# Optimization experiments

Hardware: AMD Instinct MI355X
Metric: run time of the kernel (lower is better)

## Reference

```python
import jax, jax.numpy as jnp
import numpy as np

HEADS = 4
HEAD_DIM = 32
WS = (8, 8)  # window size (h, w)


def _rel_bias_indices():
    idx = np.array([[i, j] for i in range(WS[0]) for j in range(WS[1])])  # [64,2]
    rel = idx[None, :, :] - idx[:, None, :]                               # [64,64,2]
    rel[:, :, 0] += WS[0] - 1
    rel[:, :, 1] += WS[1] - 1
    return rel

_REL = _rel_bias_indices()


def setup_inputs() -> dict:
    key = jax.random.key(0)
    ks = jax.random.split(key, 7)
    dim = 128
    inner = HEADS * HEAD_DIM
    return {
        "x": jax.random.normal(ks[0], (16, 128, 128, dim), dtype=jnp.float32),
        "w_qkv": jax.random.normal(ks[1], (dim, 3 * inner), dtype=jnp.float32) * 0.02,
        "w_out": jax.random.normal(ks[2], (inner, dim), dtype=jnp.float32) * 0.02,
        "b_out": jnp.zeros((dim,), dtype=jnp.float32),
        "pos_embedding": jax.random.normal(ks[3], (2 * WS[0] - 1, 2 * WS[1] - 1), dtype=jnp.float32) * 0.02,
        "ul_mask": jax.random.normal(ks[4], (WS[0] * WS[1], WS[0] * WS[1]), dtype=jnp.float32) * 0.02,
        "lr_mask": jax.random.normal(ks[5], (WS[0] * WS[1], WS[0] * WS[1]), dtype=jnp.float32) * 0.02,
    }


def _window_split(t, b, nw_h, nw_w):
    # (b, n_h, n_w, h*d) -> (b, h, nw, ws^2, d)
    t = t.reshape(b, nw_h, WS[0], nw_w, WS[1], HEADS, HEAD_DIM)
    t = t.transpose(0, 5, 1, 3, 2, 4, 6)
    return t.reshape(b, HEADS, nw_h * nw_w, WS[0] * WS[1], HEAD_DIM)


def reference(x, w_qkv, w_out, b_out, pos_embedding, ul_mask, lr_mask):
    b, n_h, n_w, _ = x.shape
    nw_h, nw_w = n_h // WS[0], n_w // WS[1]
    scale = HEAD_DIM ** -0.5
    disp = (WS[0] // 2, WS[1] // 2)

    # cyclic shift (torch.roll with shifts -ws//2)
    xs = jnp.roll(x, (-disp[0], -disp[1]), axis=(1, 2))

    qkv = xs @ w_qkv  # (b, n_h, n_w, 3*inner)
    q, k, v = jnp.split(qkv, 3, axis=-1)
    q = _window_split(q, b, nw_h, nw_w)
    k = _window_split(k, b, nw_h, nw_w)
    v = _window_split(v, b, nw_h, nw_w)

    dots = jnp.einsum('bhwid,bhwjd->bhwij', q, k) * scale
    bias = pos_embedding[_REL[:, :, 0], _REL[:, :, 1]]  # [64,64]
    dots = dots + bias
    # shift masks: bottom row of windows and last column of windows
    dots = dots.at[:, :, -nw_w:].add(ul_mask)
    dots = dots.at[:, :, nw_w - 1::nw_w].add(lr_mask)

    attn = jax.nn.softmax(dots, axis=-1)
    out = jnp.einsum('bhwij,bhwjd->bhwid', attn, v)

    # (b, h, nw, ws^2, d) -> (b, n_h, n_w, h*d)
    out = out.reshape(b, HEADS, nw_h, nw_w, WS[0], WS[1], HEAD_DIM)
    out = out.transpose(0, 2, 4, 3, 5, 1, 6).reshape(b, n_h, n_w, HEADS * HEAD_DIM)

    out = out @ w_out + b_out
    out = jnp.roll(out, (disp[0], disp[1]), axis=(1, 2))  # cyclic back shift
    return out
```

## Files before the change

kernel.cpp:

```cpp
#include <hip/hip_runtime.h>


typedef __bf16 bf16x8 __attribute__((ext_vector_type(8)));
typedef short  s16x8  __attribute__((ext_vector_type(8)));
typedef float  f32x4  __attribute__((ext_vector_type(4)));

static __device__ __forceinline__ float bf2f(unsigned short u) {
  unsigned x = ((unsigned)u) << 16;
  return __builtin_bit_cast(float, x);
}
static __device__ __forceinline__ unsigned short f2bf(float f) {
  unsigned x = __builtin_bit_cast(unsigned, f);
  x += 0x7FFFu + ((x >> 16) & 1u);
  return (unsigned short)(x >> 16);
}
static __device__ __forceinline__ f32x4 mfma16(s16x8 a, s16x8 b, f32x4 c) {
  return __builtin_amdgcn_mfma_f32_16x16x32_bf16(
      __builtin_bit_cast(bf16x8, a), __builtin_bit_cast(bf16x8, b), c, 0, 0, 0);
}
static __device__ __forceinline__ void bar_lds() {
  __builtin_amdgcn_sched_barrier(0);
  asm volatile("s_waitcnt lgkmcnt(0)" ::: "memory");
  __builtin_amdgcn_s_barrier();
  __builtin_amdgcn_sched_barrier(0);
}

__global__ void prep_weights(const float* __restrict__ wqkv,
                             const float* __restrict__ wout,
                             unsigned short* __restrict__ wqkvT,
                             unsigned short* __restrict__ woutT) {
  int idx = blockIdx.x * blockDim.x + threadIdx.x;
  const int total1 = 384 * 128;
  if (idx < total1) {
    int n = idx >> 7, k = idx & 127;
    wqkvT[idx] = f2bf(wqkv[k * 384 + n]);
  } else {
    int i2 = idx - total1;
    int n = i2 >> 7, k = i2 & 127;
    woutT[i2] = f2bf(wout[k * 128 + n]);
  }
}

#define OFF_XS  0
#define OFF_Q   17408
#define OFF_K   34816
#define OFF_V   52224
#define OFF_S   70656
#define OFF_OA  107520
#define OFF_BI  124928
#define SMEM_SZ 141568

#define BATCH_STRIDE (128 * 128 * 128)

__global__ __launch_bounds__(1024, 4)
void swin_fused(const float* __restrict__ x,
                const unsigned short* __restrict__ wqkvT,
                const unsigned short* __restrict__ woutT,
                const float* __restrict__ b_out,
                const float* __restrict__ pe,
                const float* __restrict__ ulm,
                const float* __restrict__ lrm,
                float* __restrict__ out) {
  __shared__ __align__(16) unsigned char smem[SMEM_SZ];
  unsigned short* xs_s   = (unsigned short*)(smem + OFF_XS);
  unsigned short* q_s    = (unsigned short*)(smem + OFF_Q);
  unsigned short* k_s    = (unsigned short*)(smem + OFF_K);
  unsigned short* v_s    = (unsigned short*)(smem + OFF_V);
  unsigned short* S_s    = (unsigned short*)(smem + OFF_S);
  float*          osr_s  = (float*)(smem + OFF_S);
  unsigned short* oa_s   = (unsigned short*)(smem + OFF_OA);
  float*          bias_s = (float*)(smem + OFF_BI);

  const int tid  = threadIdx.x;
  const int lane = tid & 63;
  const int wave = tid >> 6;
  const int ln15 = lane & 15;
  const int quad = lane >> 4;
  const int m_sub = quad << 2;

  const int wh = blockIdx.x >> 4, ww = blockIdx.x & 15;

  const int tokA = tid >> 5, c4 = tid & 31;
  const int tokB = tokA + 32;
  const int giA = ((wh << 3) + (tokA >> 3) + 4) & 127;
  const int gjA = ((ww << 3) + (tokA & 7) + 4) & 127;
  const int giB = ((wh << 3) + (tokB >> 3) + 4) & 127;
  const int gjB = ((ww << 3) + (tokB & 7) + 4) & 127;
  const long offA = (long)(giA * 128 + gjA) * 128 + c4 * 4;
  const long offB = (long)(giB * 128 + gjB) * 128 + c4 * 4;
  const float* xA = x + offA;
  const float* xB = x + offB;

  {
    float4 a0 = *(const float4*)xA;
    float4 b0 = *(const float4*)xB;
    ushort4 pk;
    pk.x = f2bf(a0.x); pk.y = f2bf(a0.y); pk.z = f2bf(a0.z); pk.w = f2bf(a0.w);
    *(ushort4*)(xs_s + tokA * 136 + c4 * 4) = pk;
    pk.x = f2bf(b0.x); pk.y = f2bf(b0.y); pk.z = f2bf(b0.z); pk.w = f2bf(b0.w);
    *(ushort4*)(xs_s + tokB * 136 + c4 * 4) = pk;

    const bool has_ul = (wh == 15), has_lr = (ww == 15);
#pragma unroll
    for (int it = 0; it < 4; ++it) {
      int t = tid + it * 1024;
      int i = t >> 6, j = t & 63;
      int r0 = (j >> 3) - (i >> 3) + 7;
      int r1 = (j & 7) - (i & 7) + 7;
      float bsum = pe[r0 * 15 + r1];
      if (has_ul) bsum += ulm[t];
      if (has_lr) bsum += lrm[t];
      bias_s[i * 65 + j] = bsum;
    }
  }
  __syncthreads();

  for (int b = 0; b < 16; ++b) {
    float4 pfA, pfB;
    const bool pf = (b < 15);
    if (pf) {
      pfA = *(const float4*)(xA + (b + 1) * BATCH_STRIDE);
      pfB = *(const float4*)(xB + (b + 1) * BATCH_STRIDE);
    }
#pragma unroll
    for (int it = 0; it < 3; ++it) {
      int t  = wave + (it << 4);
      int nt = t >> 1, mh = t & 1;
      int n0 = nt << 4;
      int n  = n0 + ln15;
      const unsigned short* wp = wqkvT + n * 128 + quad * 8;
      s16x8 bfr[4];
#pragma unroll
      for (int ks = 0; ks < 4; ++ks) bfr[ks] = *(const s16x8*)(wp + ks * 32);
#pragma unroll
      for (int mi = 0; mi < 2; ++mi) {
        int mt = mh * 2 + mi;
        f32x4 acc = {0.f, 0.f, 0.f, 0.f};
#pragma unroll
        for (int ks = 0; ks < 4; ++ks) {
          s16x8 a = *(const s16x8*)(xs_s + (mt * 16 + ln15) * 136 + ks * 32 + quad * 8);
          acc = mfma16(a, bfr[ks], acc);
        }
        int tok0 = mt * 16 + m_sub;
        if (n0 < 128) {
#pragma unroll
          for (int r = 0; r < 4; ++r) q_s[(tok0 + r) * 136 + n] = f2bf(acc[r]);
        } else if (n0 < 256) {
          int nn = n - 128;
#pragma unroll
          for (int r = 0; r < 4; ++r) k_s[(tok0 + r) * 136 + nn] = f2bf(acc[r]);
        } else {
          int nn = n - 256;
          ushort4 pk;
          pk.x = f2bf(acc[0]); pk.y = f2bf(acc[1]);
          pk.z = f2bf(acc[2]); pk.w = f2bf(acc[3]);
          *(ushort4*)(v_s + nn * 72 + tok0) = pk;
        }
      }
    }
    bar_lds();

    {
      const int h  = wave >> 2;
      const int mt = wave & 3;
      unsigned short* Sh = S_s + h * 64 * 72;
      const int tok0 = mt * 16 + m_sub;
      s16x8 qf = *(const s16x8*)(q_s + (mt * 16 + ln15) * 136 + h * 32 + quad * 8);
      const float scale = 0.17677669529663687f;
      f32x4 sv[4];
#pragma unroll
      for (int nt = 0; nt < 4; ++nt) {
        s16x8 kf = *(const s16x8*)(k_s + (nt * 16 + ln15) * 136 + h * 32 + quad * 8);
        f32x4 acc = {0.f, 0.f, 0.f, 0.f};
        acc = mfma16(qf, kf, acc);
        int nn = nt * 16 + ln15;
#pragma unroll
        for (int r = 0; r < 4; ++r)
          sv[nt][r] = acc[r] * scale + bias_s[(tok0 + r) * 65 + nn];
      }

      if (pf) {
        ushort4 pk;
        pk.x = f2bf(pfA.x); pk.y = f2bf(pfA.y); pk.z = f2bf(pfA.z); pk.w = f2bf(pfA.w);
        *(ushort4*)(xs_s + tokA * 136 + c4 * 4) = pk;
        pk.x = f2bf(pfB.x); pk.y = f2bf(pfB.y); pk.z = f2bf(pfB.z); pk.w = f2bf(pfB.w);
        *(ushort4*)(xs_s + tokB * 136 + c4 * 4) = pk;
      }

      float rinv[4];
#pragma unroll
      for (int r = 0; r < 4; ++r) {
        float m0 = fmaxf(fmaxf(sv[0][r], sv[1][r]), fmaxf(sv[2][r], sv[3][r]));
        m0 = fmaxf(m0, __shfl_xor(m0, 1));
        m0 = fmaxf(m0, __shfl_xor(m0, 2));
        m0 = fmaxf(m0, __shfl_xor(m0, 4));
        m0 = fmaxf(m0, __shfl_xor(m0, 8));
        float s0 = 0.f;
#pragma unroll
        for (int nt = 0; nt < 4; ++nt) {
          float e = __expf(sv[nt][r] - m0);
          sv[nt][r] = e;
          s0 += e;
        }
        s0 += __shfl_xor(s0, 1);
        s0 += __shfl_xor(s0, 2);
        s0 += __shfl_xor(s0, 4);
        s0 += __shfl_xor(s0, 8);
        rinv[r] = 1.0f / s0;
      }
#pragma unroll
      for (int nt = 0; nt < 4; ++nt) {
        int nn = nt * 16 + ln15;
#pragma unroll
        for (int r = 0; r < 4; ++r)
          Sh[(tok0 + r) * 72 + nn] = f2bf(sv[nt][r] * rinv[r]);
      }
      asm volatile("s_waitcnt lgkmcnt(0)" ::: "memory");
      __builtin_amdgcn_sched_barrier(0);

      s16x8 pfr[2];
#pragma unroll
      for (int ks = 0; ks < 2; ++ks)
        pfr[ks] = *(const s16x8*)(Sh + (mt * 16 + ln15) * 72 + ks * 32 + quad * 8);
#pragma unroll
      for (int nt = 0; nt < 2; ++nt) {
        f32x4 acc = {0.f, 0.f, 0.f, 0.f};
#pragma unroll
        for (int ks = 0; ks < 2; ++ks) {
          s16x8 vf = *(const s16x8*)(v_s + (h * 32 + nt * 16 + ln15) * 72 + ks * 32 + quad * 8);
          acc = mfma16(pfr[ks], vf, acc);
        }
        int n = h * 32 + nt * 16 + ln15;
#pragma unroll
        for (int r = 0; r < 4; ++r)
          oa_s[(tok0 + r) * 136 + n] = f2bf(acc[r]);
      }
    }
    bar_lds();

    {
      const int nt  = wave >> 1;
      const int mtb = (wave & 1) * 2;
      int n = nt * 16 + ln15;
      s16x8 bfr[4];
      const unsigned short* wp = woutT + n * 128 + quad * 8;
#pragma unroll
      for (int ks = 0; ks < 4; ++ks) bfr[ks] = *(const s16x8*)(wp + ks * 32);
      float bo = b_out[n];
#pragma unroll
      for (int mi = 0; mi < 2; ++mi) {
        int mt = mtb + mi;
        f32x4 acc = {0.f, 0.f, 0.f, 0.f};
#pragma unroll
        for (int ks = 0; ks < 4; ++ks) {
          s16x8 a = *(const s16x8*)(oa_s + (mt * 16 + ln15) * 136 + ks * 32 + quad * 8);
          acc = mfma16(a, bfr[ks], acc);
        }
        int tok0 = mt * 16 + m_sub;
#pragma unroll
        for (int r = 0; r < 4; ++r)
          osr_s[(tok0 + r) * 132 + n] = acc[r] + bo;
      }
    }
    bar_lds();

    {
      float* outb = out + b * BATCH_STRIDE;
      float4 o0 = *(const float4*)(osr_s + tokA * 132 + c4 * 4);
      *(float4*)(outb + offA) = o0;
      float4 o1 = *(const float4*)(osr_s + tokB * 132 + c4 * 4);
      *(float4*)(outb + offB) = o1;
    }
  }
}

extern "C" void kernel_launch(void* const* d_in, const int* in_sizes, int n_in,
                              void* d_out, int out_size, void* d_ws, size_t ws_size,
                              hipStream_t stream) {
  const float* x    = (const float*)d_in[0];
  const float* wqkv = (const float*)d_in[1];
  const float* wout = (const float*)d_in[2];
  const float* bout = (const float*)d_in[3];
  const float* pe   = (const float*)d_in[4];
  const float* ulm  = (const float*)d_in[5];
  const float* lrm  = (const float*)d_in[6];

  unsigned short* wqkvT = (unsigned short*)d_ws;
  unsigned short* woutT = wqkvT + 384 * 128;

  prep_weights<<<(384 * 128 + 128 * 128) / 256, 256, 0, stream>>>(wqkv, wout, wqkvT, woutT);
  swin_fused<<<256, 1024, 0, stream>>>(x, wqkvT, woutT, bout, pe, ulm, lrm,
                                       (float*)d_out);
}
```

Baseline: 320.8 us.

## Warp-specialize fused Swin kernel into QKV producer and attention consumer waves

Splits the 16 waves into 8 producer waves that compute the QKV projection for batch b+1 and 8 consumer waves that run attention, output projection and the store for batch b. Q/K/V buffers are double-buffered in LDS so the two stages overlap across the batch loop. Producers load x straight from global memory into MFMA fragments, dropping the LDS staging of x, and f2bf now uses the native bf16 cast. This adds LDS footprint and one extra loop iteration. Each stage now runs on half the waves, so load balance between the halves decides the outcome.

```diff
diff --git a/kernel.cpp b/kernel.cpp
--- a/kernel.cpp
+++ b/kernel.cpp
@@ -5,14 +5,17 @@
 typedef short  s16x8  __attribute__((ext_vector_type(8)));
 typedef float  f32x4  __attribute__((ext_vector_type(4)));
 
-static __device__ __forceinline__ float bf2f(unsigned short u) {
-  unsigned x = ((unsigned)u) << 16;
-  return __builtin_bit_cast(float, x);
-}
 static __device__ __forceinline__ unsigned short f2bf(float f) {
-  unsigned x = __builtin_bit_cast(unsigned, f);
-  x += 0x7FFFu + ((x >> 16) & 1u);
-  return (unsigned short)(x >> 16);
+  __bf16 h = (__bf16)f;
+  return __builtin_bit_cast(unsigned short, h);
+}
+static __device__ __forceinline__ s16x8 cvt8(float4 lo, float4 hi) {
+  s16x8 r;
+  r[0] = (short)f2bf(lo.x); r[1] = (short)f2bf(lo.y);
+  r[2] = (short)f2bf(lo.z); r[3] = (short)f2bf(lo.w);
+  r[4] = (short)f2bf(hi.x); r[5] = (short)f2bf(hi.y);
+  r[6] = (short)f2bf(hi.z); r[7] = (short)f2bf(hi.w);
+  return r;
 }
 static __device__ __forceinline__ f32x4 mfma16(s16x8 a, s16x8 b, f32x4 c) {
   return __builtin_amdgcn_mfma_f32_16x16x32_bf16(
@@ -41,16 +44,46 @@
   }
 }
 
-#define OFF_XS  0
-#define OFF_Q   17408
-#define OFF_K   34816
-#define OFF_V   52224
-#define OFF_S   70656
-#define OFF_OA  107520
-#define OFF_BI  124928
-#define SMEM_SZ 141568
+#define OFF_V0  69632
+#define OFF_PS  106496
+#define OFF_OA  124928
+#define OFF_BI  142336
+#define SMEM_SZ 158976
 
 #define BATCH_STRIDE (128 * 128 * 128)
+
+template <int KIND>
+static __device__ __forceinline__ void prod_task(
+    int nt, const s16x8 (&xf)[2][4], const unsigned short* __restrict__ wqkvT,
+    unsigned short* qw, unsigned short* kw, unsigned short* vw,
+    int ln15, int quad, int m_sub, int mh) {
+  const int n = nt * 16 + ln15;
+  const unsigned short* wp = wqkvT + n * 128 + quad * 8;
+  s16x8 bfr[4];
+#pragma unroll
+  for (int ks = 0; ks < 4; ++ks) bfr[ks] = *(const s16x8*)(wp + ks * 32);
+#pragma unroll
+  for (int mi = 0; mi < 2; ++mi) {
+    f32x4 acc = {0.f, 0.f, 0.f, 0.f};
+#pragma unroll
+    for (int ks = 0; ks < 4; ++ks) acc = mfma16(xf[mi][ks], bfr[ks], acc);
+    const int tok0 = (mh * 2 + mi) * 16 + m_sub;
+    if constexpr (KIND == 0) {
+#pragma unroll
+      for (int r = 0; r < 4; ++r) qw[(tok0 + r) * 136 + n] = f2bf(acc[r]);
+    } else if constexpr (KIND == 1) {
+      const int nn = n - 128;
+#pragma unroll
+      for (int r = 0; r < 4; ++r) kw[(tok0 + r) * 136 + nn] = f2bf(acc[r]);
+    } else {
+      const int nn = n - 256;
+      ushort4 pk;
+      pk.x = f2bf(acc[0]); pk.y = f2bf(acc[1]);
+      pk.z = f2bf(acc[2]); pk.w = f2bf(acc[3]);
+      *(ushort4*)(vw + nn * 72 + tok0) = pk;
+    }
+  }
+}
 
 __global__ __launch_bounds__(1024, 4)
 void swin_fused(const float* __restrict__ x,
@@ -62,14 +95,9 @@
                 const float* __restrict__ lrm,
                 float* __restrict__ out) {
   __shared__ __align__(16) unsigned char smem[SMEM_SZ];
-  unsigned short* xs_s   = (unsigned short*)(smem + OFF_XS);
-  unsigned short* q_s    = (unsigned short*)(smem + OFF_Q);
-  unsigned short* k_s    = (unsigned short*)(smem + OFF_K);
-  unsigned short* v_s    = (unsigned short*)(smem + OFF_V);
-  unsigned short* S_s    = (unsigned short*)(smem + OFF_S);
-  float*          osr_s  = (float*)(smem + OFF_S);
-  unsigned short* oa_s   = (unsigned short*)(smem + OFF_OA);
-  float*          bias_s = (float*)(smem + OFF_BI);
+  unsigned short* Ps_base = (unsigned short*)(smem + OFF_PS);
+  unsigned short* oa_s    = (unsigned short*)(smem + OFF_OA);
+  float*          bias_s  = (float*)(smem + OFF_BI);
 
   const int tid  = threadIdx.x;
   const int lane = tid & 63;
@@ -79,27 +107,35 @@
   const int m_sub = quad << 2;
 
   const int wh = blockIdx.x >> 4, ww = blockIdx.x & 15;
-
-  const int tokA = tid >> 5, c4 = tid & 31;
-  const int tokB = tokA + 32;
-  const int giA = ((wh << 3) + (tokA >> 3) + 4) & 127;
-  const int gjA = ((ww << 3) + (tokA & 7) + 4) & 127;
-  const int giB = ((wh << 3) + (tokB >> 3) + 4) & 127;
-  const int gjB = ((ww << 3) + (tokB & 7) + 4) & 127;
-  const long offA = (long)(giA * 128 + gjA) * 128 + c4 * 4;
-  const long offB = (long)(giB * 128 + gjB) * 128 + c4 * 4;
-  const float* xA = x + offA;
-  const float* xB = x + offB;
+  const bool is_prod = (wave < 8);
+  const int wid  = wave & 7;
+  const int cwid = wave - 8;
+
+  const int mh = wid & 1;
+  int rowoff[2];
+#pragma unroll
+  for (int mi = 0; mi < 2; ++mi) {
+    int tok = (mh * 2 + mi) * 16 + ln15;
+    int gi = ((wh << 3) + (tok >> 3) + 4) & 127;
+    int gj = ((ww << 3) + (tok & 7) + 4) & 127;
+    rowoff[mi] = (gi * 128 + gj) * 128;
+  }
+
+  int off6[4], l6[4];
+  if (!is_prod) {
+    const int ct = cwid * 64 + lane;
+#pragma unroll
+    for (int k = 0; k < 4; ++k) {
+      int item = ct + 512 * k;
+      int tok = item >> 5, c4i = item & 31;
+      int gi = ((wh << 3) + (tok >> 3) + 4) & 127;
+      int gj = ((ww << 3) + (tok & 7) + 4) & 127;
+      off6[k] = (gi * 128 + gj) * 128 + c4i * 4;
+      l6[k] = tok * 132 + c4i * 4;
+    }
+  }
 
   {
-    float4 a0 = *(const float4*)xA;
-    float4 b0 = *(const float4*)xB;
-    ushort4 pk;
-    pk.x = f2bf(a0.x); pk.y = f2bf(a0.y); pk.z = f2bf(a0.z); pk.w = f2bf(a0.w);
-    *(ushort4*)(xs_s + tokA * 136 + c4 * 4) = pk;
-    pk.x = f2bf(b0.x); pk.y = f2bf(b0.y); pk.z = f2bf(b0.z); pk.w = f2bf(b0.w);
-    *(ushort4*)(xs_s + tokB * 136 + c4 * 4) = pk;
-
     const bool has_ul = (wh == 15), has_lr = (ww == 15);
 #pragma unroll
     for (int it = 0; it < 4; ++it) {
@@ -115,162 +151,146 @@
   }
   __syncthreads();
 
-  for (int b = 0; b < 16; ++b) {
-    float4 pfA, pfB;
-    const bool pf = (b < 15);
-    if (pf) {
-      pfA = *(const float4*)(xA + (b + 1) * BATCH_STRIDE);
-      pfB = *(const float4*)(xB + (b + 1) * BATCH_STRIDE);
-    }
-#pragma unroll
-    for (int it = 0; it < 3; ++it) {
-      int t  = wave + (it << 4);
-      int nt = t >> 1, mh = t & 1;
-      int n0 = nt << 4;
-      int n  = n0 + ln15;
-      const unsigned short* wp = wqkvT + n * 128 + quad * 8;
-      s16x8 bfr[4];
-#pragma unroll
-      for (int ks = 0; ks < 4; ++ks) bfr[ks] = *(const s16x8*)(wp + ks * 32);
-#pragma unroll
-      for (int mi = 0; mi < 2; ++mi) {
-        int mt = mh * 2 + mi;
+  int wbuf = 1;
+  for (int b = -1; b < 16; ++b) {
+    const int rbuf = wbuf ^ 1;
+    unsigned short* qw = (unsigned short*)(smem + wbuf * 34816);
+    unsigned short* kw = qw + 8704;
+    unsigned short* vw = (unsigned short*)(smem + OFF_V0 + wbuf * 18432);
+    unsigned short* qr = (unsigned short*)(smem + rbuf * 34816);
+    unsigned short* kr = qr + 8704;
+    unsigned short* vr = (unsigned short*)(smem + OFF_V0 + rbuf * 18432);
+    float*          osr = (float*)(smem + rbuf * 34816);
+
+    const int nb = b + 1;
+    const bool do_p = is_prod && (nb < 16);
+    const bool do_c = (!is_prod) && (b >= 0);
+
+    s16x8 xf[2][4];
+    if (do_p) {
+      const float* xb = x + (long)nb * BATCH_STRIDE;
+#pragma unroll
+      for (int mi = 0; mi < 2; ++mi)
+#pragma unroll
+        for (int ks = 0; ks < 4; ++ks) {
+          const float* p = xb + rowoff[mi] + ks * 32 + quad * 8;
+          float4 lo = *(const float4*)p;
+          float4 hi = *(const float4*)(p + 4);
+          xf[mi][ks] = cvt8(lo, hi);
+        }
+      prod_task<0>(wid >> 1,     xf, wqkvT, qw, kw, vw, ln15, quad, m_sub, mh);
+      prod_task<0>((wid >> 1)+4, xf, wqkvT, qw, kw, vw, ln15, quad, m_sub, mh);
+    } else if (do_c) {
+      unsigned short* Ps = Ps_base + cwid * 1152;
+      const int mt = cwid & 3;
+      const int tok0 = mt * 16 + m_sub;
+      const float scale = 0.17677669529663687f;
+#pragma unroll
+      for (int i = 0; i < 2; ++i) {
+        const int h = (cwid >> 2) + 2 * i;
+        s16x8 qf = *(const s16x8*)(qr + (mt * 16 + ln15) * 136 + h * 32 + quad * 8);
+        f32x4 sv[4];
+#pragma unroll
+        for (int nt = 0; nt < 4; ++nt) {
+          s16x8 kf = *(const s16x8*)(kr + (nt * 16 + ln15) * 136 + h * 32 + quad * 8);
+          f32x4 acc = {0.f, 0.f, 0.f, 0.f};
+          acc = mfma16(qf, kf, acc);
+          int nn = nt * 16 + ln15;
+#pragma unroll
+          for (int r = 0; r < 4; ++r)
+            sv[nt][r] = acc[r] * scale + bias_s[(tok0 + r) * 65 + nn];
+        }
+        float rinv[4];
+#pragma unroll
+        for (int r = 0; r < 4; ++r) {
+          float m0 = fmaxf(fmaxf(sv[0][r], sv[1][r]), fmaxf(sv[2][r], sv[3][r]));
+          m0 = fmaxf(m0, __shfl_xor(m0, 1));
+          m0 = fmaxf(m0, __shfl_xor(m0, 2));
+          m0 = fmaxf(m0, __shfl_xor(m0, 4));
+          m0 = fmaxf(m0, __shfl_xor(m0, 8));
+          float s0 = 0.f;
+#pragma unroll
+          for (int nt = 0; nt < 4; ++nt) {
+            float e = __expf(sv[nt][r] - m0);
+            sv[nt][r] = e;
+            s0 += e;
+          }
+          s0 += __shfl_xor(s0, 1);
+          s0 += __shfl_xor(s0, 2);
+          s0 += __shfl_xor(s0, 4);
+          s0 += __shfl_xor(s0, 8);
+          rinv[r] = 1.0f / s0;
+        }
+#pragma unroll
+        for (int nt = 0; nt < 4; ++nt) {
+          int nn = nt * 16 + ln15;
+#pragma unroll
+          for (int r = 0; r < 4; ++r)
+            Ps[(m_sub + r) * 72 + nn] = f2bf(sv[nt][r] * rinv[r]);
+        }
+        asm volatile("s_waitcnt lgkmcnt(0)" ::: "memory");
+        __builtin_amdgcn_sched_barrier(0);
+        s16x8 pfr[2];
+#pragma unroll
+        for (int ks = 0; ks < 2; ++ks)
+          pfr[ks] = *(const s16x8*)(Ps + ln15 * 72 + ks * 32 + quad * 8);
+#pragma unroll
+        for (int nt2 = 0; nt2 < 2; ++nt2) {
+          f32x4 acc = {0.f, 0.f, 0.f, 0.f};
+#pragma unroll
+          for (int ks = 0; ks < 2; ++ks) {
+            s16x8 vf = *(const s16x8*)(vr + (h * 32 + nt2 * 16 + ln15) * 72 + ks * 32 + quad * 8);
+            acc = mfma16(pfr[ks], vf, acc);
+          }
+          int n = h * 32 + nt2 * 16 + ln15;
+#pragma unroll
+          for (int r = 0; r < 4; ++r)
+            oa_s[(tok0 + r) * 136 + n] = f2bf(acc[r]);
+        }
+      }
+    }
+    bar_lds();
+
+    if (do_p) {
+      prod_task<1>((wid >> 1) + 8,  xf, wqkvT, qw, kw, vw, ln15, quad, m_sub, mh);
+      prod_task<1>((wid >> 1) + 12, xf, wqkvT, qw, kw, vw, ln15, quad, m_sub, mh);
+    } else if (do_c) {
+      const int mt5 = cwid >> 1, nh = cwid & 1;
+      s16x8 af[4];
+#pragma unroll
+      for (int ks = 0; ks < 4; ++ks)
+        af[ks] = *(const s16x8*)(oa_s + (mt5 * 16 + ln15) * 136 + ks * 32 + quad * 8);
+#pragma unroll
+      for (int nt = 0; nt < 4; ++nt) {
+        int n = nh * 64 + nt * 16 + ln15;
+        const unsigned short* wp = woutT + n * 128 + quad * 8;
+        s16x8 bfr[4];
+#pragma unroll
+        for (int ks = 0; ks < 4; ++ks) bfr[ks] = *(const s16x8*)(wp + ks * 32);
         f32x4 acc = {0.f, 0.f, 0.f, 0.f};
 #pragma unroll
-        for (int ks = 0; ks < 4; ++ks) {
-          s16x8 a = *(const s16x8*)(xs_s + (mt * 16 + ln15) * 136 + ks * 32 + quad * 8);
-          acc = mfma16(a, bfr[ks], acc);
-        }
-        int tok0 = mt * 16 + m_sub;
-        if (n0 < 128) {
-#pragma unroll
-          for (int r = 0; r < 4; ++r) q_s[(tok0 + r) * 136 + n] = f2bf(acc[r]);
-        } else if (n0 < 256) {
-          int nn = n - 128;
-#pragma unroll
-          for (int r = 0; r < 4; ++r) k_s[(tok0 + r) * 136 + nn] = f2bf(acc[r]);
-        } else {
-          int nn = n - 256;
-          ushort4 pk;
-          pk.x = f2bf(acc[0]); pk.y = f2bf(acc[1]);
-          pk.z = f2bf(acc[2]); pk.w = f2bf(acc[3]);
-          *(ushort4*)(v_s + nn * 72 + tok0) = pk;
-        }
+        for (int ks = 0; ks < 4; ++ks) acc = mfma16(af[ks], bfr[ks], acc);
+        float bo = b_out[n];
+#pragma unroll
+        for (int r = 0; r < 4; ++r)
+          osr[(mt5 * 16 + m_sub + r) * 132 + n] = acc[r] + bo;
       }
     }
     bar_lds();
 
-    {
-      const int h  = wave >> 2;
-      const int mt = wave & 3;
-      unsigned short* Sh = S_s + h * 64 * 72;
-      const int tok0 = mt * 16 + m_sub;
-      s16x8 qf = *(const s16x8*)(q_s + (mt * 16 + ln15) * 136 + h * 32 + quad * 8);
-      const float scale = 0.17677669529663687f;
-      f32x4 sv[4];
-#pragma unroll
-      for (int nt = 0; nt < 4; ++nt) {
-        s16x8 kf = *(const s16x8*)(k_s + (nt * 16 + ln15) * 136 + h * 32 + quad * 8);
-        f32x4 acc = {0.f, 0.f, 0.f, 0.f};
-        acc = mfma16(qf, kf, acc);
-        int nn = nt * 16 + ln15;
-#pragma unroll
-        for (int r = 0; r < 4; ++r)
-          sv[nt][r] = acc[r] * scale + bias_s[(tok0 + r) * 65 + nn];
+    if (do_p) {
+      prod_task<2>((wid >> 1) + 16, xf, wqkvT, qw, kw, vw, ln15, quad, m_sub, mh);
+      prod_task<2>((wid >> 1) + 20, xf, wqkvT, qw, kw, vw, ln15, quad, m_sub, mh);
+    } else if (do_c) {
+      float* outb = out + (long)b * BATCH_STRIDE;
+#pragma unroll
+      for (int k = 0; k < 4; ++k) {
+        float4 o = *(const float4*)(osr + l6[k]);
+        *(float4*)(outb + off6[k]) = o;
       }
-
-      if (pf) {
-        ushort4 pk;
-        pk.x = f2bf(pfA.x); pk.y = f2bf(pfA.y); pk.z = f2bf(pfA.z); pk.w = f2bf(pfA.w);
-        *(ushort4*)(xs_s + tokA * 136 + c4 * 4) = pk;
-        pk.x = f2bf(pfB.x); pk.y = f2bf(pfB.y); pk.z = f2bf(pfB.z); pk.w = f2bf(pfB.w);
-        *(ushort4*)(xs_s + tokB * 136 + c4 * 4) = pk;
-      }
-
-      float rinv[4];
-#pragma unroll
-      for (int r = 0; r < 4; ++r) {
-        float m0 = fmaxf(fmaxf(sv[0][r], sv[1][r]), fmaxf(sv[2][r], sv[3][r]));
-        m0 = fmaxf(m0, __shfl_xor(m0, 1));
-        m0 = fmaxf(m0, __shfl_xor(m0, 2));
-        m0 = fmaxf(m0, __shfl_xor(m0, 4));
-        m0 = fmaxf(m0, __shfl_xor(m0, 8));
-        float s0 = 0.f;
-#pragma unroll
-        for (int nt = 0; nt < 4; ++nt) {
-          float e = __expf(sv[nt][r] - m0);
-          sv[nt][r] = e;
-          s0 += e;
-        }
-        s0 += __shfl_xor(s0, 1);
-        s0 += __shfl_xor(s0, 2);
-        s0 += __shfl_xor(s0, 4);
-        s0 += __shfl_xor(s0, 8);
-        rinv[r] = 1.0f / s0;
-      }
-#pragma unroll
-      for (int nt = 0; nt < 4; ++nt) {
-        int nn = nt * 16 + ln15;
-#pragma unroll
-        for (int r = 0; r < 4; ++r)
-          Sh[(tok0 + r) * 72 + nn] = f2bf(sv[nt][r] * rinv[r]);
-      }
-      asm volatile("s_waitcnt lgkmcnt(0)" ::: "memory");
-      __builtin_amdgcn_sched_barrier(0);
-
-      s16x8 pfr[2];
-#pragma unroll
-      for (int ks = 0; ks < 2; ++ks)
-        pfr[ks] = *(const s16x8*)(Sh + (mt * 16 + ln15) * 72 + ks * 32 + quad * 8);
-#pragma unroll
-      for (int nt = 0; nt < 2; ++nt) {
-        f32x4 acc = {0.f, 0.f, 0.f, 0.f};
-#pragma unroll
-        for (int ks = 0; ks < 2; ++ks) {
-          s16x8 vf = *(const s16x8*)(v_s + (h * 32 + nt * 16 + ln15) * 72 + ks * 32 + quad * 8);
-          acc = mfma16(pfr[ks], vf, acc);
-        }
-        int n = h * 32 + nt * 16 + ln15;
-#pragma unroll
-        for (int r = 0; r < 4; ++r)
-          oa_s[(tok0 + r) * 136 + n] = f2bf(acc[r]);
-      }
     }
     bar_lds();
-
-    {
-      const int nt  = wave >> 1;
-      const int mtb = (wave & 1) * 2;
-      int n = nt * 16 + ln15;
-      s16x8 bfr[4];
-      const unsigned short* wp = woutT + n * 128 + quad * 8;
-#pragma unroll
-      for (int ks = 0; ks < 4; ++ks) bfr[ks] = *(const s16x8*)(wp + ks * 32);
-      float bo = b_out[n];
-#pragma unroll
-      for (int mi = 0; mi < 2; ++mi) {
-        int mt = mtb + mi;
-        f32x4 acc = {0.f, 0.f, 0.f, 0.f};
-#pragma unroll
-        for (int ks = 0; ks < 4; ++ks) {
-          s16x8 a = *(const s16x8*)(oa_s + (mt * 16 + ln15) * 136 + ks * 32 + quad * 8);
-          acc = mfma16(a, bfr[ks], acc);
-        }
-        int tok0 = mt * 16 + m_sub;
-#pragma unroll
-        for (int r = 0; r < 4; ++r)
-          osr_s[(tok0 + r) * 132 + n] = acc[r] + bo;
-      }
-    }
-    bar_lds();
-
-    {
-      float* outb = out + b * BATCH_STRIDE;
-      float4 o0 = *(const float4*)(osr_s + tokA * 132 + c4 * 4);
-      *(float4*)(outb + offA) = o0;
-      float4 o1 = *(const float4*)(osr_s + tokB * 132 + c4 * 4);
-      *(float4*)(outb + offB) = o1;
-    }
+    wbuf = rbuf;
   }
 }
 
```

Result: slower. 428.9 us (+33.7%).
